# Optimization experiments

Measured on AMD Instinct MI355X. Metric: run time of the kernel, lower is better.

Reference implementation:

```python
import jax, jax.numpy as jnp
import numpy as np

B, N, K, C_IN, OC = 16, 4096, 16, 64, 64
OC2 = OC // 2
LEAK = 0.2
EPS = 1e-12  # guards sqrt grad when a neighbor equals the center point


def _cbn(x, w, s, b):
    # 1x1 conv (channel-last) + folded eval-mode BatchNorm: (x @ w.T) * s + b
    return jnp.einsum('...i,oi->...o', x, w) * s + b


def _lrelu(x):
    return jax.nn.leaky_relu(x, LEAK)


def _gather(feat, idx):
    # feat [B,N,C], idx [B,N,k] -> [B,N,k,C]  (index_points)
    return jax.vmap(lambda f, i: f[i])(feat, idx)


def _attentive_pool(x_info, feat, idx, wq, sq, bq, wk, sk, bk, wv, sv, bv, w2, s2, b2):
    q = jax.nn.relu(_cbn(feat, wq, sq, bq))   # [B,N,C]
    kf = jax.nn.relu(_cbn(feat, wk, sk, bk))
    vf = jax.nn.relu(_cbn(feat, wv, sv, bv))
    Kn = _gather(kf, idx)                     # [B,N,k,C]
    W = x_info * (Kn - q[:, :, None, :])      # [B,N,k,C]
    Vn = _gather(vf, idx)
    a = jax.nn.softmax(W, axis=2)             # softmax over k neighbors
    out = jnp.sum(a * Vn, axis=2)             # [B,N,C]
    return _lrelu(_cbn(out, w2, s2, b2))


def _forward(x, feature, neighbor_index,
             mlp1_w, mlp1_s, mlp1_b, lse1_w, lse1_s, lse1_b,
             p1_wq, p1_sq, p1_bq, p1_wk, p1_sk, p1_bk, p1_wv, p1_sv, p1_bv, p1_w2, p1_s2, p1_b2,
             lse2_w, lse2_s, lse2_b,
             p2_wq, p2_sq, p2_bq, p2_wk, p2_sk, p2_bk, p2_wv, p2_sv, p2_bv, p2_w2, p2_s2, p2_b2,
             mlp2_w, mlp2_s, mlp2_b, res_w, res_s, res_b):
    idx = neighbor_index
    xt = jnp.transpose(x, (0, 2, 1))          # [B,N,3]
    ft = jnp.transpose(feature, (0, 2, 1))    # [B,N,C_IN]
    identity = ft
    f1 = _lrelu(_cbn(ft, mlp1_w, mlp1_s, mlp1_b))        # [B,N,OC2]
    knn_x = _gather(xt, idx)                             # [B,N,k,3]
    center = jnp.broadcast_to(xt[:, :, None, :], knn_x.shape)
    diff = knn_x - center
    dist = jnp.sqrt(jnp.sum(diff * diff, axis=-1, keepdims=True) + EPS)  # [B,N,k,1]
    x_info = jnp.concatenate([center, knn_x, diff, dist], axis=-1)       # [B,N,k,10]
    x_info = _lrelu(_cbn(x_info, lse1_w, lse1_s, lse1_b))                # [B,N,k,OC2]
    feat2 = _attentive_pool(x_info, f1, idx,
                            p1_wq, p1_sq, p1_bq, p1_wk, p1_sk, p1_bk,
                            p1_wv, p1_sv, p1_bv, p1_w2, p1_s2, p1_b2)    # [B,N,OC2]
    x_info2 = _lrelu(_cbn(x_info, lse2_w, lse2_s, lse2_b))               # [B,N,k,OC2]
    feat3 = _attentive_pool(x_info2, feat2, idx,
                            p2_wq, p2_sq, p2_bq, p2_wk, p2_sk, p2_bk,
                            p2_wv, p2_sv, p2_bv, p2_w2, p2_s2, p2_b2)    # [B,N,OC]
    out = _cbn(feat3, mlp2_w, mlp2_s, mlp2_b)            # [B,N,2*OC]
    res = _cbn(identity, res_w, res_s, res_b)            # [B,N,2*OC]
    out = _lrelu(out + res)
    return jnp.transpose(out, (0, 2, 1))                 # [B,2*OC,N]


def setup_inputs() -> dict:
    key = jax.random.key(0)
    it = iter(jax.random.split(key, 80))
    nxt = lambda: next(it)

    def w(*shape):
        return jax.random.normal(nxt(), shape, jnp.float32) * 0.1

    def bn(c):
        s = jax.random.uniform(nxt(), (c,), jnp.float32, 0.5, 1.5)
        b = jax.random.normal(nxt(), (c,), jnp.float32) * 0.1
        return s, b

    inp = {
        'x': jax.random.normal(nxt(), (B, 3, N), jnp.float32),
        'feature': jax.random.normal(nxt(), (B, C_IN, N), jnp.float32),
        'neighbor_index': jax.random.randint(nxt(), (B, N, K), 0, N, jnp.int32),
    }
    inp['mlp1_w'] = w(OC2, C_IN); inp['mlp1_s'], inp['mlp1_b'] = bn(OC2)
    inp['lse1_w'] = w(OC2, 10); inp['lse1_s'], inp['lse1_b'] = bn(OC2)
    for p, co in (('p1', OC2), ('p2', OC)):
        inp[p + '_wq'] = w(OC2, OC2); inp[p + '_sq'], inp[p + '_bq'] = bn(OC2)
        inp[p + '_wk'] = w(OC2, OC2); inp[p + '_sk'], inp[p + '_bk'] = bn(OC2)
        inp[p + '_wv'] = w(OC2, OC2); inp[p + '_sv'], inp[p + '_bv'] = bn(OC2)
        inp[p + '_w2'] = w(co, OC2); inp[p + '_s2'], inp[p + '_b2'] = bn(co)
    inp['lse2_w'] = w(OC2, OC2); inp['lse2_s'], inp['lse2_b'] = bn(OC2)
    inp['mlp2_w'] = w(2 * OC, OC); inp['mlp2_s'], inp['mlp2_b'] = bn(2 * OC)
    inp['res_w'] = w(2 * OC, C_IN); inp['res_s'], inp['res_b'] = bn(2 * OC)
    return inp


def reference(x, feature, neighbor_index,
              mlp1_w, mlp1_s, mlp1_b, lse1_w, lse1_s, lse1_b,
              p1_wq, p1_sq, p1_bq, p1_wk, p1_sk, p1_bk, p1_wv, p1_sv, p1_bv, p1_w2, p1_s2, p1_b2,
              lse2_w, lse2_s, lse2_b,
              p2_wq, p2_sq, p2_bq, p2_wk, p2_sk, p2_bk, p2_wv, p2_sv, p2_bv, p2_w2, p2_s2, p2_b2,
              mlp2_w, mlp2_s, mlp2_b, res_w, res_s, res_b):
    return _forward(x, feature, neighbor_index,
                    mlp1_w, mlp1_s, mlp1_b, lse1_w, lse1_s, lse1_b,
                    p1_wq, p1_sq, p1_bq, p1_wk, p1_sk, p1_bk, p1_wv, p1_sv, p1_bv, p1_w2, p1_s2, p1_b2,
                    lse2_w, lse2_s, lse2_b,
                    p2_wq, p2_sq, p2_bq, p2_wk, p2_sk, p2_bk, p2_wv, p2_sv, p2_bv, p2_w2, p2_s2, p2_b2,
                    mlp2_w, mlp2_s, mlp2_b, res_w, res_s, res_b)
```

## Files before the change

kernel.cpp:

```cpp
#include <hip/hip_runtime.h>
#include <cstdint>
#include <cstddef>

#define NB 16
#define NP 4096
#define KNN 16
#define CIN 64
#define H 32
#define OCC 64
#define PN ((size_t)NB*NP)

__device__ __forceinline__ float lrelu(float v){ return v > 0.f ? v : 0.2f*v; }
__device__ __forceinline__ float reluf(float v){ return v > 0.f ? v : 0.f; }

typedef __attribute__((ext_vector_type(8)))  short bf16x8s;
typedef __attribute__((ext_vector_type(4)))  float f32x4;
typedef __attribute__((ext_vector_type(16))) float f32x16;

__device__ __forceinline__ short f2bf(float f){
    union { float f; unsigned u; } v; v.f = f;
    unsigned r = v.u + 0x7fffu + ((v.u >> 16) & 1u);
    return (short)(r >> 16);
}

__device__ __forceinline__ bf16x8s pack8(float4 a, float4 b, float sc){
    bf16x8s r;
    r[0]=f2bf(a.x*sc); r[1]=f2bf(a.y*sc); r[2]=f2bf(a.z*sc); r[3]=f2bf(a.w*sc);
    r[4]=f2bf(b.x*sc); r[5]=f2bf(b.y*sc); r[6]=f2bf(b.z*sc); r[7]=f2bf(b.w*sc);
    return r;
}

__global__ __launch_bounds__(256) void k_pointwise(
    const float* __restrict__ feat, const float* __restrict__ xpos,
    const float* __restrict__ w1, const float* __restrict__ s1, const float* __restrict__ b1,
    const float* __restrict__ wq, const float* __restrict__ sq, const float* __restrict__ bq,
    const float* __restrict__ wk, const float* __restrict__ sk, const float* __restrict__ bk,
    const float* __restrict__ wv, const float* __restrict__ sv, const float* __restrict__ bv,
    float* __restrict__ q1, float* __restrict__ kv1,
    float* __restrict__ xp, float* __restrict__ ftp)
{
    __shared__ float ftile[CIN][65];
    __shared__ float f1t[H][65];
    int t = threadIdx.x;
    int l = t & 63;
    int g = __builtin_amdgcn_readfirstlane(t >> 6);
    int bid = blockIdx.x;
    int b  = bid >> 6;
    int n0 = (bid & 63) * 64;
    int n  = n0 + l;
    size_t p = (size_t)b*NP + n;

    const float* fb = feat + ((size_t)b*CIN)*NP + n;
    float fv[16];
    #pragma unroll
    for (int k=0;k<16;k++){
        int c = g*16 + k;
        fv[k] = fb[(size_t)c*NP];
        ftile[c][l] = fv[k];
    }
    #pragma unroll
    for (int k4=0;k4<4;k4++)
        *(float4*)(ftp + p*64 + g*16 + k4*4) =
            make_float4(fv[k4*4],fv[k4*4+1],fv[k4*4+2],fv[k4*4+3]);
    if (g == 0){
        const float* xb = xpos + (size_t)b*3*NP;
        *(float4*)(xp + 4*p) = make_float4(xb[n], xb[NP+n], xb[2*NP+n], 0.f);
    }
    __syncthreads();

    float acc[8];
    #pragma unroll
    for (int u=0;u<8;u++) acc[u] = 0.f;
    #pragma unroll
    for (int c=0;c<CIN;c++){
        float x = ftile[c][l];
        #pragma unroll
        for (int u=0;u<8;u++) acc[u] = fmaf(w1[(g*8+u)*CIN+c], x, acc[u]);
    }
    #pragma unroll
    for (int u=0;u<8;u++){
        int h = g*8+u;
        f1t[h][l] = lrelu(acc[u]*s1[h] + b1[h]);
    }
    __syncthreads();

    float aq[8], ak[8], av[8];
    #pragma unroll
    for (int u=0;u<8;u++){ aq[u]=0.f; ak[u]=0.f; av[u]=0.f; }
    #pragma unroll
    for (int j=0;j<H;j++){
        float x = f1t[j][l];
        #pragma unroll
        for (int u=0;u<8;u++){
            int h = g*8+u;
            aq[u] = fmaf(wq[h*H+j], x, aq[u]);
            ak[u] = fmaf(wk[h*H+j], x, ak[u]);
            av[u] = fmaf(wv[h*H+j], x, av[u]);
        }
    }
    float qr[8], kr[8], vr[8];
    #pragma unroll
    for (int u=0;u<8;u++){
        int h = g*8+u;
        qr[u] = reluf(aq[u]*sq[h]+bq[h]);
        kr[u] = reluf(ak[u]*sk[h]+bk[h]);
        vr[u] = reluf(av[u]*sv[h]+bv[h]);
    }
    size_t qb = p*H + g*8;
    *(float4*)(q1+qb)   = make_float4(qr[0],qr[1],qr[2],qr[3]);
    *(float4*)(q1+qb+4) = make_float4(qr[4],qr[5],qr[6],qr[7]);
    size_t kb = (p*H + g*8)*2;
    #pragma unroll
    for (int u2=0;u2<4;u2++)
        *(float4*)(kv1+kb+u2*4) = make_float4(kr[u2*2],vr[u2*2],kr[u2*2+1],vr[u2*2+1]);
}

__global__ __launch_bounds__(256) void k_pool1(
    const float* __restrict__ xp, const int* __restrict__ nidx,
    const float* __restrict__ q1, const float* __restrict__ kv1,
    const float* __restrict__ l1w, const float* __restrict__ l1s, const float* __restrict__ l1b,
    const float* __restrict__ w2, const float* __restrict__ s2, const float* __restrict__ b2,
    const float* __restrict__ wq, const float* __restrict__ sq, const float* __restrict__ bq,
    const float* __restrict__ wk, const float* __restrict__ sk, const float* __restrict__ bk,
    const float* __restrict__ wv, const float* __restrict__ sv, const float* __restrict__ bv,
    float* __restrict__ q2, float* __restrict__ kv2)
{
    __shared__ float wl[4][32*36];
    __shared__ float bcp[4][2][32];
    __shared__ float bcf[4][2][32];
    int t = threadIdx.x;
    {
        const float* wsrc[4] = {w2, wq, wk, wv};
        #pragma unroll
        for (int m=0;m<4;m++)
            for (int i=t;i<1024;i+=256)
                wl[m][(i>>5)*36 + (i&31)] = wsrc[m][i];
    }
    __syncthreads();

    int wv_ = t >> 6;
    int l   = t & 63;
    int n_  = l & 31;
    int hi  = l >> 5;
    size_t p0 = (size_t)blockIdx.x*8 + (size_t)wv_*2;
    int b = (int)(p0 >> 12);

    bf16x8s Bf;
    if (hi == 0){
        #pragma unroll
        for (int i=0;i<8;i++) Bf[i] = f2bf(l1w[n_*10 + i]);
    } else {
        Bf[0] = f2bf(l1w[n_*10 + 8]);
        Bf[1] = f2bf(l1w[n_*10 + 9]);
        #pragma unroll
        for (int i=2;i<8;i++) Bf[i] = 0;
    }

    int ptA  = (l >> 4) & 1;
    int nbrA = l & 15;
    size_t pA = p0 + ptA;
    int idA = nidx[pA*KNN + nbrA];
    float4 cp = *(const float4*)(xp + 4*pA);
    float4 nv = *(const float4*)(xp + 4*((size_t)(b<<12)+idA));
    float dx = nv.x-cp.x, dy = nv.y-cp.y, dz = nv.z-cp.z;
    float dist = sqrtf(dx*dx+dy*dy+dz*dz + 1e-12f);
    bf16x8s A;
    if (hi == 0){
        A[0]=f2bf(cp.x); A[1]=f2bf(cp.y); A[2]=f2bf(cp.z); A[3]=f2bf(nv.x);
        A[4]=f2bf(nv.y); A[5]=f2bf(nv.z); A[6]=f2bf(dx);   A[7]=f2bf(dy);
    } else {
        A[0]=f2bf(dz); A[1]=f2bf(dist);
        A[2]=0; A[3]=0; A[4]=0; A[5]=0; A[6]=0; A[7]=0;
    }

    f32x16 cz = {0.f,0.f,0.f,0.f,0.f,0.f,0.f,0.f,0.f,0.f,0.f,0.f,0.f,0.f,0.f,0.f};
    f32x16 D = __builtin_amdgcn_mfma_f32_32x32x16_bf16(A, Bf, cz, 0, 0, 0);

    float sl1 = l1s[n_], bl1 = l1b[n_];
    const int* irow0 = nidx + p0*KNN;
    float outv[2];
    #pragma unroll
    for (int pt=0; pt<2; pt++){
        size_t p = p0 + pt;
        float qc = q1[p*H + n_];
        int4 idlo = *(const int4*)(irow0 + pt*KNN + 4*hi);
        int4 idhi = *(const int4*)(irow0 + pt*KNN + 8 + 4*hi);
        int ids[8] = {idlo.x,idlo.y,idlo.z,idlo.w, idhi.x,idhi.y,idhi.z,idhi.w};
        float W[8], V[8];
        #pragma unroll
        for (int rr=0; rr<8; rr++){
            float xi = lrelu(D[pt*8+rr]*sl1 + bl1);
            float2 kv = *(const float2*)(kv1 + 2*(((size_t)b*NP + ids[rr])*H + n_));
            W[rr] = xi*(kv.x - qc);
            V[rr] = kv.y;
        }
        float mx = W[0];
        #pragma unroll
        for (int rr=1;rr<8;rr++) mx = fmaxf(mx, W[rr]);
        mx = fmaxf(mx, __shfl_xor(mx, 32, 64));
        float den = 0.f, ac = 0.f;
        #pragma unroll
        for (int rr=0;rr<8;rr++){
            float e = __expf(W[rr]-mx);
            den += e; ac = fmaf(e, V[rr], ac);
        }
        den += __shfl_xor(den, 32, 64);
        ac  += __shfl_xor(ac,  32, 64);
        outv[pt] = ac/den;
    }
    if (l < 32){ bcp[wv_][0][n_] = outv[0]; bcp[wv_][1][n_] = outv[1]; }

    int c = n_;
    float f2a = 0.f;
    #pragma unroll
    for (int jj=0;jj<8;jj++){
        float4 xv = *(const float4*)&bcp[wv_][hi][jj*4];
        float4 w4 = *(const float4*)&wl[0][c*36 + jj*4];
        f2a += w4.x*xv.x + w4.y*xv.y + w4.z*xv.z + w4.w*xv.w;
    }
    float f2 = lrelu(f2a*s2[c] + b2[c]);
    bcf[wv_][hi][c] = f2;

    float aq=0.f, ak=0.f, av=0.f;
    #pragma unroll
    for (int jj=0;jj<8;jj++){
        float4 xv  = *(const float4*)&bcf[wv_][hi][jj*4];
        float4 wq4 = *(const float4*)&wl[1][c*36 + jj*4];
        float4 wk4 = *(const float4*)&wl[2][c*36 + jj*4];
        float4 wv4 = *(const float4*)&wl[3][c*36 + jj*4];
        aq += wq4.x*xv.x + wq4.y*xv.y + wq4.z*xv.z + wq4.w*xv.w;
        ak += wk4.x*xv.x + wk4.y*xv.y + wk4.z*xv.z + wk4.w*xv.w;
        av += wv4.x*xv.x + wv4.y*xv.y + wv4.z*xv.z + wv4.w*xv.w;
    }
    size_t base = (p0 + hi)*H + c;
    q2[base] = reluf(aq*sq[c]+bq[c]);
    *(float2*)(kv2 + 2*base) = make_float2(reluf(ak*sk[c]+bk[c]), reluf(av*sv[c]+bv[c]));
}

__global__ __launch_bounds__(256) void k_pool2(
    const float* __restrict__ xp, const int* __restrict__ nidx,
    const float* __restrict__ q2, const float* __restrict__ kv2,
    const float* __restrict__ l1w, const float* __restrict__ l1s, const float* __restrict__ l1b,
    const float* __restrict__ l2w, const float* __restrict__ l2s, const float* __restrict__ l2b,
    const float* __restrict__ w2, const float* __restrict__ s2, const float* __restrict__ b2,
    float* __restrict__ f3)
{
    __shared__ float wt1[10][32];
    __shared__ float we[64*36];
    __shared__ float bc[4][2][32];
    int t = threadIdx.x;
    if (t < 320) wt1[t>>5][t&31] = l1w[(t&31)*10 + (t>>5)];
    for (int i=t;i<2048;i+=256) we[(i>>5)*36 + (i&31)] = w2[i];
    __syncthreads();

    int wv_ = t >> 6;
    int l   = t & 63;
    int n_  = l & 31;
    int hi  = l >> 5;
    size_t p0 = (size_t)blockIdx.x*8 + (size_t)wv_*2;
    int b = (int)(p0 >> 12);

    int ptA  = (l >> 4) & 1;
    int nbrA = l & 15;
    size_t pA = p0 + ptA;
    int idA = nidx[pA*KNN + nbrA];
    float4 cp = *(const float4*)(xp + 4*pA);
    float4 nv = *(const float4*)(xp + 4*((size_t)(b<<12)+idA));
    float dx = nv.x-cp.x, dy = nv.y-cp.y, dz = nv.z-cp.z;
    float dist = sqrtf(dx*dx+dy*dy+dz*dz + 1e-12f);
    float gv[10] = {cp.x,cp.y,cp.z,nv.x,nv.y,nv.z,dx,dy,dz,dist};

    int ch0 = hi*8;
    float xa[8] = {0,0,0,0,0,0,0,0}, xb2[8] = {0,0,0,0,0,0,0,0};
    #pragma unroll
    for (int j=0;j<10;j++){
        float g = gv[j];
        float4 wA = *(const float4*)&wt1[j][ch0];
        float4 wB = *(const float4*)&wt1[j][ch0+4];
        float4 wC = *(const float4*)&wt1[j][16+ch0];
        float4 wD = *(const float4*)&wt1[j][16+ch0+4];
        xa[0]=fmaf(wA.x,g,xa[0]); xa[1]=fmaf(wA.y,g,xa[1]);
        xa[2]=fmaf(wA.z,g,xa[2]); xa[3]=fmaf(wA.w,g,xa[3]);
        xa[4]=fmaf(wB.x,g,xa[4]); xa[5]=fmaf(wB.y,g,xa[5]);
        xa[6]=fmaf(wB.z,g,xa[6]); xa[7]=fmaf(wB.w,g,xa[7]);
        xb2[0]=fmaf(wC.x,g,xb2[0]); xb2[1]=fmaf(wC.y,g,xb2[1]);
        xb2[2]=fmaf(wC.z,g,xb2[2]); xb2[3]=fmaf(wC.w,g,xb2[3]);
        xb2[4]=fmaf(wD.x,g,xb2[4]); xb2[5]=fmaf(wD.y,g,xb2[5]);
        xb2[6]=fmaf(wD.z,g,xb2[6]); xb2[7]=fmaf(wD.w,g,xb2[7]);
    }
    float4 s1a = *(const float4*)(l1s + ch0), s1b = *(const float4*)(l1s + ch0 + 4);
    float4 s1c = *(const float4*)(l1s + 16 + ch0), s1d = *(const float4*)(l1s + 16 + ch0 + 4);
    float4 b1a = *(const float4*)(l1b + ch0), b1b = *(const float4*)(l1b + ch0 + 4);
    float4 b1c = *(const float4*)(l1b + 16 + ch0), b1d = *(const float4*)(l1b + 16 + ch0 + 4);
    bf16x8s A0, A1;
    A0[0]=f2bf(lrelu(xa[0]*s1a.x+b1a.x)); A0[1]=f2bf(lrelu(xa[1]*s1a.y+b1a.y));
    A0[2]=f2bf(lrelu(xa[2]*s1a.z+b1a.z)); A0[3]=f2bf(lrelu(xa[3]*s1a.w+b1a.w));
    A0[4]=f2bf(lrelu(xa[4]*s1b.x+b1b.x)); A0[5]=f2bf(lrelu(xa[5]*s1b.y+b1b.y));
    A0[6]=f2bf(lrelu(xa[6]*s1b.z+b1b.z)); A0[7]=f2bf(lrelu(xa[7]*s1b.w+b1b.w));
    A1[0]=f2bf(lrelu(xb2[0]*s1c.x+b1c.x)); A1[1]=f2bf(lrelu(xb2[1]*s1c.y+b1c.y));
    A1[2]=f2bf(lrelu(xb2[2]*s1c.z+b1c.z)); A1[3]=f2bf(lrelu(xb2[3]*s1c.w+b1c.w));
    A1[4]=f2bf(lrelu(xb2[4]*s1d.x+b1d.x)); A1[5]=f2bf(lrelu(xb2[5]*s1d.y+b1d.y));
    A1[6]=f2bf(lrelu(xb2[6]*s1d.z+b1d.z)); A1[7]=f2bf(lrelu(xb2[7]*s1d.w+b1d.w));

    bf16x8s B0, B1;
    {
        const float* r0 = l2w + n_*32 + ch0;
        #pragma unroll
        for (int i=0;i<8;i++){ B0[i] = f2bf(r0[i]); B1[i] = f2bf(r0[16+i]); }
    }

    f32x16 cz = {0.f,0.f,0.f,0.f,0.f,0.f,0.f,0.f,0.f,0.f,0.f,0.f,0.f,0.f,0.f,0.f};
    f32x16 D = __builtin_amdgcn_mfma_f32_32x32x16_bf16(A0, B0, cz, 0, 0, 0);
    D = __builtin_amdgcn_mfma_f32_32x32x16_bf16(A1, B1, D, 0, 0, 0);

    float sl2 = l2s[n_], bl2 = l2b[n_];
    const int* irow0 = nidx + p0*KNN;
    float outv[2];
    #pragma unroll
    for (int pt=0; pt<2; pt++){
        size_t p = p0 + pt;
        float qc = q2[p*H + n_];
        int4 idlo = *(const int4*)(irow0 + pt*KNN + 4*hi);
        int4 idhi = *(const int4*)(irow0 + pt*KNN + 8 + 4*hi);
        int ids[8] = {idlo.x,idlo.y,idlo.z,idlo.w, idhi.x,idhi.y,idhi.z,idhi.w};
        float W[8], V[8];
        #pragma unroll
        for (int rr=0; rr<8; rr++){
            float xi2 = lrelu(D[pt*8+rr]*sl2 + bl2);
            float2 kv = *(const float2*)(kv2 + 2*(((size_t)b*NP + ids[rr])*H + n_));
            W[rr] = xi2*(kv.x - qc);
            V[rr] = kv.y;
        }
        float mx = W[0];
        #pragma unroll
        for (int rr=1;rr<8;rr++) mx = fmaxf(mx, W[rr]);
        mx = fmaxf(mx, __shfl_xor(mx, 32, 64));
        float den = 0.f, ac = 0.f;
        #pragma unroll
        for (int rr=0;rr<8;rr++){
            float e = __expf(W[rr]-mx);
            den += e; ac = fmaf(e, V[rr], ac);
        }
        den += __shfl_xor(den, 32, 64);
        ac  += __shfl_xor(ac,  32, 64);
        outv[pt] = ac/den;
    }
    if (l < 32){ bc[wv_][0][n_] = outv[0]; bc[wv_][1][n_] = outv[1]; }

    float fa=0.f, fb2=0.f;
    #pragma unroll
    for (int jj=0;jj<8;jj++){
        float4 xv  = *(const float4*)&bc[wv_][hi][jj*4];
        float4 wa4 = *(const float4*)&we[n_*36 + jj*4];
        float4 wb4 = *(const float4*)&we[(n_+32)*36 + jj*4];
        fa  += wa4.x*xv.x + wa4.y*xv.y + wa4.z*xv.z + wa4.w*xv.w;
        fb2 += wb4.x*xv.x + wb4.y*xv.y + wb4.z*xv.z + wb4.w*xv.w;
    }
    size_t pp = p0 + hi;
    f3[pp*64 + n_]      = lrelu(fa *s2[n_]    + b2[n_]);
    f3[pp*64 + 32 + n_] = lrelu(fb2*s2[n_+32] + b2[n_+32]);
}

__global__ __launch_bounds__(256) void k_final(
    const float* __restrict__ ftp, const float* __restrict__ f3,
    const float* __restrict__ m2w, const float* __restrict__ m2s, const float* __restrict__ m2b,
    const float* __restrict__ rw, const float* __restrict__ rs, const float* __restrict__ rb,
    float* __restrict__ out)
{
    int t = threadIdx.x;
    int l  = t & 63;
    int w  = t >> 6;
    int lr = l & 15;
    int lg = l >> 4;
    int ot0 = w * 32;

    bf16x8s A[2][4];
    float bias[2][4];
    #pragma unroll
    for (int mt=0; mt<2; mt++){
        int o = ot0 + mt*16 + lr;
        float scm = m2s[o], scr = rs[o];
        const float* pm = m2w + (size_t)o*64 + lg*8;
        const float* pr = rw  + (size_t)o*64 + lg*8;
        #pragma unroll
        for (int kk=0;kk<2;kk++)
            A[mt][kk] = pack8(*(const float4*)(pm + kk*32),
                              *(const float4*)(pm + kk*32 + 4), scm);
        #pragma unroll
        for (int kk=0;kk<2;kk++)
            A[mt][2+kk] = pack8(*(const float4*)(pr + kk*32),
                                *(const float4*)(pr + kk*32 + 4), scr);
        int od = ot0 + mt*16 + lg*4;
        #pragma unroll
        for (int r=0;r<4;r++) bias[mt][r] = m2b[od+r] + rb[od+r];
    }

    size_t pbase = (size_t)blockIdx.x * 64;
    int b = (int)(pbase >> 12);
    float* ob = out + ((size_t)b*128)*NP;

    #pragma unroll
    for (int ti=0; ti<4; ti++){
        size_t p0 = pbase + ti*16;
        int n0 = (int)(p0 & (NP-1));
        size_t prow = (p0 + lr)*64 + lg*8;
        bf16x8s Bf[4];
        #pragma unroll
        for (int kk=0;kk<2;kk++)
            Bf[kk] = pack8(*(const float4*)(f3 + prow + kk*32),
                           *(const float4*)(f3 + prow + kk*32 + 4), 1.f);
        #pragma unroll
        for (int kk=0;kk<2;kk++)
            Bf[2+kk] = pack8(*(const float4*)(ftp + prow + kk*32),
                             *(const float4*)(ftp + prow + kk*32 + 4), 1.f);
        #pragma unroll
        for (int mt=0;mt<2;mt++){
            f32x4 D = {0.f,0.f,0.f,0.f};
            #pragma unroll
            for (int kk=0;kk<4;kk++)
                D = __builtin_amdgcn_mfma_f32_16x16x32_bf16(A[mt][kk], Bf[kk], D, 0, 0, 0);
            #pragma unroll
            for (int r=0;r<4;r++){
                int od = ot0 + mt*16 + lg*4 + r;
                ob[(size_t)od*NP + n0 + lr] = lrelu(D[r] + bias[mt][r]);
            }
        }
    }
}

extern "C" void kernel_launch(void* const* d_in, const int* in_sizes, int n_in,
                              void* d_out, int out_size, void* d_ws, size_t ws_size,
                              hipStream_t stream)
{
    (void)in_sizes; (void)n_in; (void)out_size; (void)ws_size;
    const float* x     = (const float*)d_in[0];
    const float* feat  = (const float*)d_in[1];
    const int*   nidx  = (const int*)  d_in[2];
    const float* m1w=(const float*)d_in[3],  *m1s=(const float*)d_in[4],  *m1b=(const float*)d_in[5];
    const float* l1w=(const float*)d_in[6],  *l1s=(const float*)d_in[7],  *l1b=(const float*)d_in[8];
    const float* p1wq=(const float*)d_in[9],  *p1sq=(const float*)d_in[10], *p1bq=(const float*)d_in[11];
    const float* p1wk=(const float*)d_in[12], *p1sk=(const float*)d_in[13], *p1bk=(const float*)d_in[14];
    const float* p1wv=(const float*)d_in[15], *p1sv=(const float*)d_in[16], *p1bv=(const float*)d_in[17];
    const float* p1w2=(const float*)d_in[18], *p1s2=(const float*)d_in[19], *p1b2=(const float*)d_in[20];
    const float* p2wq=(const float*)d_in[21], *p2sq=(const float*)d_in[22], *p2bq=(const float*)d_in[23];
    const float* p2wk=(const float*)d_in[24], *p2sk=(const float*)d_in[25], *p2bk=(const float*)d_in[26];
    const float* p2wv=(const float*)d_in[27], *p2sv=(const float*)d_in[28], *p2bv=(const float*)d_in[29];
    const float* p2w2=(const float*)d_in[30], *p2s2=(const float*)d_in[31], *p2b2=(const float*)d_in[32];
    const float* l2w=(const float*)d_in[33], *l2s=(const float*)d_in[34], *l2b=(const float*)d_in[35];
    const float* m2w=(const float*)d_in[36], *m2s=(const float*)d_in[37], *m2b=(const float*)d_in[38];
    const float* rw =(const float*)d_in[39], *rs =(const float*)d_in[40], *rb =(const float*)d_in[41];

    float* ws = (float*)d_ws;
    float* q1  = ws;
    float* kv1 = ws + PN*32;
    float* q2  = ws + PN*96;
    float* kv2 = ws + PN*128;
    float* xp  = ws + PN*192;
    float* ftp = ws + PN*196;
    float* f3  = ws;

    float* outp = (float*)d_out;

    k_pointwise<<<dim3(PN/64),dim3(256),0,stream>>>(feat, x, m1w,m1s,m1b,
        p1wq,p1sq,p1bq, p1wk,p1sk,p1bk, p1wv,p1sv,p1bv, q1,kv1, xp, ftp);
    k_pool1<<<dim3(PN/8),dim3(256),0,stream>>>(xp,nidx, q1,kv1,
        l1w,l1s,l1b, p1w2,p1s2,p1b2,
        p2wq,p2sq,p2bq, p2wk,p2sk,p2bk, p2wv,p2sv,p2bv, q2,kv2);
    k_pool2<<<dim3(PN/8),dim3(256),0,stream>>>(xp,nidx, q2,kv2,
        l1w,l1s,l1b, l2w,l2s,l2b, p2w2,p2s2,p2b2, f3);
    k_final<<<dim3(PN/64),dim3(256),0,stream>>>(ftp, f3, m2w,m2s,m2b, rw,rs,rb, outp);
}
```

Before: 325.9 us.

## Store ftp and f3 intermediates as bf16 and swizzle pool block order

The transposed input features and the pool2 output are now written to workspace as bf16 rather than fp32, so k_final loads MFMA operands directly with no conversion, and the intermediate traffic is halved. The pool kernels also remap block indices so consecutive blocks are spread across batches, which changes which blocks run concurrently and may affect cache or channel locality. Rounding moves earlier in the pipeline but matches what k_final already did before its MFMA.

```diff
diff --git a/kernel.cpp b/kernel.cpp
--- a/kernel.cpp
+++ b/kernel.cpp
@@ -37,7 +37,7 @@
     const float* __restrict__ wk, const float* __restrict__ sk, const float* __restrict__ bk,
     const float* __restrict__ wv, const float* __restrict__ sv, const float* __restrict__ bv,
     float* __restrict__ q1, float* __restrict__ kv1,
-    float* __restrict__ xp, float* __restrict__ ftp)
+    float* __restrict__ xp, short* __restrict__ ftp)
 {
     __shared__ float ftile[CIN][65];
     __shared__ float f1t[H][65];
@@ -58,10 +58,13 @@
         fv[k] = fb[(size_t)c*NP];
         ftile[c][l] = fv[k];
     }
-    #pragma unroll
-    for (int k4=0;k4<4;k4++)
-        *(float4*)(ftp + p*64 + g*16 + k4*4) =
-            make_float4(fv[k4*4],fv[k4*4+1],fv[k4*4+2],fv[k4*4+3]);
+    {
+        bf16x8s h0, h1;
+        #pragma unroll
+        for (int i=0;i<8;i++){ h0[i] = f2bf(fv[i]); h1[i] = f2bf(fv[8+i]); }
+        *(bf16x8s*)(ftp + p*64 + g*16)     = h0;
+        *(bf16x8s*)(ftp + p*64 + g*16 + 8) = h1;
+    }
     if (g == 0){
         const float* xb = xpos + (size_t)b*3*NP;
         *(float4*)(xp + 4*p) = make_float4(xb[n], xb[NP+n], xb[2*NP+n], 0.f);
@@ -142,7 +145,9 @@
     int l   = t & 63;
     int n_  = l & 31;
     int hi  = l >> 5;
-    size_t p0 = (size_t)blockIdx.x*8 + (size_t)wv_*2;
+    int bid = blockIdx.x;
+    int sb  = ((bid & 7) << 10) | (bid >> 3);
+    size_t p0 = (size_t)sb*8 + (size_t)wv_*2;
     int b = (int)(p0 >> 12);
 
     bf16x8s Bf;
@@ -243,7 +248,7 @@
     const float* __restrict__ l1w, const float* __restrict__ l1s, const float* __restrict__ l1b,
     const float* __restrict__ l2w, const float* __restrict__ l2s, const float* __restrict__ l2b,
     const float* __restrict__ w2, const float* __restrict__ s2, const float* __restrict__ b2,
-    float* __restrict__ f3)
+    short* __restrict__ f3)
 {
     __shared__ float wt1[10][32];
     __shared__ float we[64*36];
@@ -257,7 +262,9 @@
     int l   = t & 63;
     int n_  = l & 31;
     int hi  = l >> 5;
-    size_t p0 = (size_t)blockIdx.x*8 + (size_t)wv_*2;
+    int bid = blockIdx.x;
+    int sb  = ((bid & 7) << 10) | (bid >> 3);
+    size_t p0 = (size_t)sb*8 + (size_t)wv_*2;
     int b = (int)(p0 >> 12);
 
     int ptA  = (l >> 4) & 1;
@@ -357,12 +364,12 @@
         fb2 += wb4.x*xv.x + wb4.y*xv.y + wb4.z*xv.z + wb4.w*xv.w;
     }
     size_t pp = p0 + hi;
-    f3[pp*64 + n_]      = lrelu(fa *s2[n_]    + b2[n_]);
-    f3[pp*64 + 32 + n_] = lrelu(fb2*s2[n_+32] + b2[n_+32]);
+    f3[pp*64 + n_]      = f2bf(lrelu(fa *s2[n_]    + b2[n_]));
+    f3[pp*64 + 32 + n_] = f2bf(lrelu(fb2*s2[n_+32] + b2[n_+32]));
 }
 
 __global__ __launch_bounds__(256) void k_final(
-    const float* __restrict__ ftp, const float* __restrict__ f3,
+    const short* __restrict__ ftp, const short* __restrict__ f3,
     const float* __restrict__ m2w, const float* __restrict__ m2s, const float* __restrict__ m2b,
     const float* __restrict__ rw, const float* __restrict__ rs, const float* __restrict__ rb,
     float* __restrict__ out)
@@ -403,16 +410,13 @@
     for (int ti=0; ti<4; ti++){
         size_t p0 = pbase + ti*16;
         int n0 = (int)(p0 & (NP-1));
-        size_t prow = (p0 + lr)*64 + lg*8;
+        const short* fp3 = f3  + (p0 + lr)*64 + lg*8;
+        const short* fpt = ftp + (p0 + lr)*64 + lg*8;
         bf16x8s Bf[4];
-        #pragma unroll
-        for (int kk=0;kk<2;kk++)
-            Bf[kk] = pack8(*(const float4*)(f3 + prow + kk*32),
-                           *(const float4*)(f3 + prow + kk*32 + 4), 1.f);
-        #pragma unroll
-        for (int kk=0;kk<2;kk++)
-            Bf[2+kk] = pack8(*(const float4*)(ftp + prow + kk*32),
-                             *(const float4*)(ftp + prow + kk*32 + 4), 1.f);
+        Bf[0] = *(const bf16x8s*)(fp3);
+        Bf[1] = *(const bf16x8s*)(fp3 + 32);
+        Bf[2] = *(const bf16x8s*)(fpt);
+        Bf[3] = *(const bf16x8s*)(fpt + 32);
         #pragma unroll
         for (int mt=0;mt<2;mt++){
             f32x4 D = {0.f,0.f,0.f,0.f};
@@ -456,8 +460,8 @@
     float* q2  = ws + PN*96;
     float* kv2 = ws + PN*128;
     float* xp  = ws + PN*192;
-    float* ftp = ws + PN*196;
-    float* f3  = ws;
+    short* ftp = (short*)(ws + PN*196);
+    short* f3  = (short*)ws;
 
     float* outp = (float*)d_out;
 
```

New measurement: 308.9 us. 5.2% less time.
